# Kernel optimization log

Hardware: AMD Instinct MI355X
Metric: run time of the kernel (lower is better)

Reference implementation:

```python
import jax, jax.numpy as jnp
import numpy as np


def setup_inputs() -> dict:
    key = jax.random.key(0)
    k1, k2, k3, k4, k5 = jax.random.split(key, 5)
    B, T, U, D = 4, 256, 64, 512
    H, V = 512, 1024  # forward_output_size, num_classes
    return {
        "encoder_outputs": jax.random.normal(k1, (B, T, D), dtype=jnp.float32),
        "decoder_outputs": jax.random.normal(k2, (B, U, D), dtype=jnp.float32),
        "w1": jax.random.normal(k3, (H, 2 * D), dtype=jnp.float32) * 0.02,
        "b1": jax.random.normal(k4, (H,), dtype=jnp.float32) * 0.02,
        "w2": jax.random.normal(k5, (V, H), dtype=jnp.float32) * 0.02,
    }


def reference(encoder_outputs, decoder_outputs, w1, b1, w2):
    # Faithful to: concat([enc broadcast to (B,T,U,D), dec broadcast to (B,T,U,D)], -1)
    # -> Linear(w1,b1) -> GELU(tanh) -> Linear(w2, no bias).
    # Linear on the concat equals split-weight projections summed via broadcast
    # (classic RNNT joint decomposition): same math, avoids the (B,T,U,2D) tensor.
    D = encoder_outputs.shape[-1]
    w_enc, w_dec = w1[:, :D], w1[:, D:]
    enc_proj = jnp.einsum("btd,hd->bth", encoder_outputs, w_enc)  # (B,T,H)
    dec_proj = jnp.einsum("bud,hd->buh", decoder_outputs, w_dec)  # (B,U,H)
    hidden = enc_proj[:, :, None, :] + dec_proj[:, None, :, :] + b1  # (B,T,U,H)
    hidden = jax.nn.gelu(hidden, approximate=True)  # tanh approximation, matches nn.GELU('tanh')
    logits = jnp.einsum("btuh,vh->btuv", hidden, w2)  # (B,T,U,V)
    return logits
```

## Files before the change

kernel.cpp:

```cpp
#include <hip/hip_runtime.h>
#include <hip/hip_bf16.h>
#include <stdint.h>


typedef __bf16 bf16_t;
typedef bf16_t bf16x8 __attribute__((ext_vector_type(8)));
typedef float f32x4 __attribute__((ext_vector_type(4)));
typedef unsigned short u16x8 __attribute__((ext_vector_type(8)));

#define GLD16(gp, lp)                                                          \
  __builtin_amdgcn_global_load_lds(                                            \
      (const __attribute__((address_space(1))) void*)(gp),                     \
      (__attribute__((address_space(3))) void*)(lp), 16, 0, 0)

__device__ __forceinline__ unsigned short f2bf(float f) {
  unsigned int u = __float_as_uint(f);
  return (unsigned short)((u + 0x7FFFu + ((u >> 16) & 1u)) >> 16);
}

__device__ __forceinline__ float gelu_f(float x) {
  float t = 1.5957691216057308f * x + 0.07135481283867141f * (x * x * x);
  float e = __expf(-t);
  return x * __builtin_amdgcn_rcpf(1.0f + e);
}

__global__ __launch_bounds__(256) void prep_kernel(
    const float* __restrict__ enc, const float* __restrict__ dec,
    const float* __restrict__ w1, const float* __restrict__ w2,
    unsigned short* __restrict__ o) {
  int i = (blockIdx.x * 256 + threadIdx.x) * 4;
  float4 v;
  if (i < 524288) {
    v = *(const float4*)(enc + i);
  } else if (i < 655360) {
    v = *(const float4*)(dec + (i - 524288));
  } else if (i < 917504) {
    int j = i - 655360;
    v = *(const float4*)(w1 + (j >> 9) * 1024 + (j & 511));
  } else if (i < 1179648) {
    int j = i - 917504;
    v = *(const float4*)(w1 + (j >> 9) * 1024 + 512 + (j & 511));
  } else {
    v = *(const float4*)(w2 + (i - 1179648));
  }
  ushort4 r;
  r.x = f2bf(v.x); r.y = f2bf(v.y); r.z = f2bf(v.z); r.w = f2bf(v.w);
  *(ushort4*)(o + i) = r;
}

__global__ __launch_bounds__(256) void hidden_kernel(
    const float* __restrict__ ep, const float* __restrict__ dp,
    const float* __restrict__ b1, unsigned short* __restrict__ o) {
  int g = blockIdx.x * 256 + threadIdx.x;
  int m = g >> 6;
  int h = (g & 63) << 3;
  int er = m >> 6;
  int dr = ((m >> 14) << 6) | (m & 63);
  float4 e0 = *(const float4*)(ep + er * 512 + h);
  float4 e1 = *(const float4*)(ep + er * 512 + h + 4);
  float4 d0 = *(const float4*)(dp + dr * 512 + h);
  float4 d1 = *(const float4*)(dp + dr * 512 + h + 4);
  float4 b0 = *(const float4*)(b1 + h);
  float4 b1v = *(const float4*)(b1 + h + 4);
  u16x8 r;
  r[0] = f2bf(gelu_f(e0.x + d0.x + b0.x));
  r[1] = f2bf(gelu_f(e0.y + d0.y + b0.y));
  r[2] = f2bf(gelu_f(e0.z + d0.z + b0.z));
  r[3] = f2bf(gelu_f(e0.w + d0.w + b0.w));
  r[4] = f2bf(gelu_f(e1.x + d1.x + b1v.x));
  r[5] = f2bf(gelu_f(e1.y + d1.y + b1v.y));
  r[6] = f2bf(gelu_f(e1.z + d1.z + b1v.z));
  r[7] = f2bf(gelu_f(e1.w + d1.w + b1v.w));
  *(u16x8*)(o + (size_t)g * 8) = r;
}

__device__ __forceinline__ void gemm_core(
    const bf16_t* __restrict__ A, const bf16_t* __restrict__ B,
    float* __restrict__ C, int m0, int n0, int N, int K) {
  __shared__ bf16_t sA[128 * 64];
  __shared__ bf16_t sB[128 * 64];

  const int tid = threadIdx.x;
  const int lane = tid & 63;
  const int w = tid >> 6;
  const int wm = (w >> 1) * 64;
  const int wn = (w & 1) * 64;

  const int srow = w * 32 + (lane >> 3);
  const int scol = (((lane & 7) ^ (lane >> 3)) << 3);
  const bf16_t* gA = A + (size_t)(m0 + srow) * K + scol;
  const bf16_t* gB = B + (size_t)(n0 + srow) * K + scol;

  const int rowA = wm + (lane & 15);
  const int rowB = wn + (lane & 15);
  const int sw0 = (lane >> 4) ^ (lane & 7);
  const bf16x8* pA = (const bf16x8*)sA;
  const bf16x8* pB = (const bf16x8*)sB;

  f32x4 acc[4][4] = {};

  for (int kt = 0; kt < K; kt += 64) {
#pragma unroll
    for (int j = 0; j < 4; j++) {
      GLD16(gA + (size_t)(j * 8) * K + kt, sA + (w * 4 + j) * 512);
      GLD16(gB + (size_t)(j * 8) * K + kt, sB + (w * 4 + j) * 512);
    }
    __syncthreads();

#pragma unroll
    for (int kk = 0; kk < 2; kk++) {
      const int sw = sw0 ^ (kk << 2);
      bf16x8 af[4], bb[4];
#pragma unroll
      for (int i = 0; i < 4; i++) af[i] = pA[(rowA + i * 16) * 8 + sw];
#pragma unroll
      for (int j = 0; j < 4; j++) bb[j] = pB[(rowB + j * 16) * 8 + sw];
#pragma unroll
      for (int i = 0; i < 4; i++)
#pragma unroll
        for (int j = 0; j < 4; j++)
          acc[i][j] = __builtin_amdgcn_mfma_f32_16x16x32_bf16(
              af[i], bb[j], acc[i][j], 0, 0, 0);
    }
    __syncthreads();
  }

  const int crow = m0 + wm + (lane >> 4) * 4;
  const int ccol = n0 + wn + (lane & 15);
  float* Cp = C + (size_t)crow * N + ccol;
#pragma unroll
  for (int i = 0; i < 4; i++)
#pragma unroll
    for (int r = 0; r < 4; r++)
#pragma unroll
      for (int j = 0; j < 4; j++)
        Cp[(size_t)(i * 16 + r) * N + j * 16] = acc[i][j][r];
}

__global__ __launch_bounds__(256) void proj_kernel(
    const bf16_t* __restrict__ encA, const bf16_t* __restrict__ wenc,
    float* __restrict__ encC, const bf16_t* __restrict__ decA,
    const bf16_t* __restrict__ wdec, float* __restrict__ decC) {
  int by = blockIdx.y;
  if (by < 8) {
    gemm_core(encA, wenc, encC, by * 128, blockIdx.x * 128, 512, 512);
  } else {
    gemm_core(decA, wdec, decC, (by - 8) * 128, blockIdx.x * 128, 512, 512);
  }
}


#define STG_A(BUF, RH, KT)                                                     \
  do {                                                                         \
    GLD16(gA + (size_t)((RH) * 64) * 512 + (KT) * 64,                          \
          &sA[BUF][(RH) * 64 + w * 8][0]);                                     \
    GLD16(gA + (size_t)((RH) * 64 + 128) * 512 + (KT) * 64,                    \
          &sA[BUF][(RH) * 64 + 128 + w * 8][0]);                               \
  } while (0)

#define STG_B(BUF, H, KT)                                                      \
  do {                                                                         \
    GLD16(gB + (size_t)((H) * 128) * 512 + (KT) * 64,                          \
          &sB[BUF][(H) * 128 + w * 16][0]);                                    \
    GLD16(gB + (size_t)((H) * 128 + 8) * 512 + (KT) * 64,                      \
          &sB[BUF][(H) * 128 + w * 16 + 8][0]);                                \
  } while (0)

#define RD_A(BUF, F, KK)                                                       \
  pA[(BUF) * 2048 + (rowA + (F) * 16) * 8 + (sw0 ^ ((KK) << 2))]
#define RD_B(BUF, ROFF, KK)                                                    \
  pB[(BUF) * 2048 + (rowB + (ROFF)) * 8 + (sw0 ^ ((KK) << 2))]

#define VMC4 asm volatile("s_waitcnt vmcnt(4)" ::: "memory")
#define VMC0 asm volatile("s_waitcnt vmcnt(0)" ::: "memory")
#define NOPX ((void)0)

#define PHASE(BUF, RH, CH, STAGE, VM)                                          \
  do {                                                                         \
    if ((CH) == 0) {                                                           \
      _Pragma("unroll") for (int f = 0; f < 4; f++) {                          \
        af[f][0] = RD_A(BUF, (RH) * 4 + f, 0);                                 \
        af[f][1] = RD_A(BUF, (RH) * 4 + f, 1);                                 \
      }                                                                        \
    }                                                                          \
    _Pragma("unroll") for (int cf = 0; cf < 2; cf++) {                         \
      bb[cf][0] = RD_B(BUF, (CH) * 128 + cf * 16, 0);                          \
      bb[cf][1] = RD_B(BUF, (CH) * 128 + cf * 16, 1);                          \
    }                                                                          \
    STAGE;                                                                     \
    VM;                                                                        \
    __builtin_amdgcn_s_barrier();                                              \
    __builtin_amdgcn_s_setprio(1);                                             \
    _Pragma("unroll") for (int f = 0; f < 4; f++) {                            \
      _Pragma("unroll") for (int cf = 0; cf < 2; cf++) {                       \
        acc[(RH) * 4 + f][(CH) * 2 + cf] =                                     \
            __builtin_amdgcn_mfma_f32_16x16x32_bf16(                           \
                af[f][0], bb[cf][0], acc[(RH) * 4 + f][(CH) * 2 + cf], 0, 0,   \
                0);                                                            \
        acc[(RH) * 4 + f][(CH) * 2 + cf] =                                     \
            __builtin_amdgcn_mfma_f32_16x16x32_bf16(                           \
                af[f][1], bb[cf][1], acc[(RH) * 4 + f][(CH) * 2 + cf], 0, 0,   \
                0);                                                            \
      }                                                                        \
    }                                                                          \
    __builtin_amdgcn_s_setprio(0);                                             \
    __builtin_amdgcn_s_barrier();                                              \
  } while (0)

__global__ __launch_bounds__(512, 2) void gemm_big2(
    const bf16_t* __restrict__ A, const bf16_t* __restrict__ B,
    float* __restrict__ C) {
  __shared__ bf16_t sA[2][256][64];
  __shared__ bf16_t sB[2][256][64];

  const int tid = threadIdx.x;
  const int lane = tid & 63;
  const int w = tid >> 6;
  const int wr = w >> 2;
  const int wc = w & 3;

  const int bid = blockIdx.x;
  const int swz = (bid & 7) * 128 + (bid >> 3);
  const int m0 = (swz >> 2) * 256;
  const int n0 = (swz & 3) * 256;

  const int srowA = w * 8 + (lane >> 3);
  const int srowB = w * 16 + (lane >> 3);
  const int scol = ((lane & 7) ^ (lane >> 3)) << 3;
  const bf16_t* gA = A + (size_t)(m0 + srowA) * 512 + scol;
  const bf16_t* gB = B + (size_t)(n0 + srowB) * 512 + scol;

  const int rowA = wr * 128 + (lane & 15);
  const int rowB = wc * 32 + (lane & 15);
  const int sw0 = (lane >> 4) ^ (lane & 7);
  const bf16x8* pA = (const bf16x8*)sA;
  const bf16x8* pB = (const bf16x8*)sB;

  f32x4 acc[8][4] = {};
  bf16x8 af[4][2], bb[2][2];

  STG_A(0, 0, 0); STG_B(0, 0, 0); STG_A(0, 1, 0); STG_B(0, 1, 0);
  STG_A(1, 0, 1); STG_B(1, 0, 1);
  VMC4;
  __builtin_amdgcn_s_barrier();

#pragma unroll 1
  for (int i = 0; i < 3; i++) {
    const int t1k = 2 * i + 1;
    const int t2k = 2 * i + 2;
    const int t3k = 2 * i + 3;
    PHASE(0, 0, 0, STG_A(1, 1, t1k), NOPX);
    PHASE(0, 0, 1, STG_B(1, 1, t1k), NOPX);
    PHASE(0, 1, 0, STG_A(0, 0, t2k), NOPX);
    PHASE(0, 1, 1, STG_B(0, 0, t2k), VMC4);
    PHASE(1, 0, 0, STG_A(0, 1, t2k), NOPX);
    PHASE(1, 0, 1, STG_B(0, 1, t2k), NOPX);
    PHASE(1, 1, 0, STG_A(1, 0, t3k), NOPX);
    PHASE(1, 1, 1, STG_B(1, 0, t3k), VMC4);
  }
  PHASE(0, 0, 0, STG_A(1, 1, 7), NOPX);
  PHASE(0, 0, 1, STG_B(1, 1, 7), NOPX);
  PHASE(0, 1, 0, NOPX, NOPX);
  PHASE(0, 1, 1, NOPX, VMC0);
  PHASE(1, 0, 0, NOPX, NOPX);
  PHASE(1, 0, 1, NOPX, NOPX);
  PHASE(1, 1, 0, NOPX, NOPX);
  PHASE(1, 1, 1, NOPX, NOPX);

  const int crow = m0 + wr * 128 + (lane >> 4) * 4;
  const int ccol = n0 + wc * 32 + (lane & 15);
  float* Cp = C + (size_t)crow * 1024 + ccol;
#pragma unroll
  for (int f = 0; f < 8; f++)
#pragma unroll
    for (int r = 0; r < 4; r++)
#pragma unroll
      for (int c = 0; c < 4; c++)
        Cp[(size_t)(f * 16 + r) * 1024 + (c >> 1) * 128 + (c & 1) * 16] =
            acc[f][c][r];
}

extern "C" void kernel_launch(void* const* d_in, const int* in_sizes, int n_in,
                              void* d_out, int out_size, void* d_ws,
                              size_t ws_size, hipStream_t stream) {
  const float* enc = (const float*)d_in[0];
  const float* dec = (const float*)d_in[1];
  const float* w1  = (const float*)d_in[2];
  const float* b1  = (const float*)d_in[3];
  const float* w2  = (const float*)d_in[4];
  float* out = (float*)d_out;

  unsigned short* bf      = (unsigned short*)d_ws;
  unsigned short* ws_enc  = bf;
  unsigned short* ws_dec  = bf + 524288;
  unsigned short* ws_wenc = bf + 655360;
  unsigned short* ws_wdec = bf + 917504;
  unsigned short* ws_w2   = bf + 1179648;
  float* encp = (float*)((char*)d_ws + 3407872);
  float* decp = encp + 524288;
  unsigned short* hid = (unsigned short*)(decp + 131072);

  prep_kernel<<<1664, 256, 0, stream>>>(enc, dec, w1, w2, bf);

  proj_kernel<<<dim3(4, 10), 256, 0, stream>>>(
      (const bf16_t*)ws_enc, (const bf16_t*)ws_wenc, encp,
      (const bf16_t*)ws_dec, (const bf16_t*)ws_wdec, decp);

  hidden_kernel<<<16384, 256, 0, stream>>>(encp, decp, b1, hid);

  gemm_big2<<<1024, 512, 0, stream>>>(
      (const bf16_t*)hid, (const bf16_t*)ws_w2, out);
}
```

Before: 362.4 us.

## Fuse broadcast-add GELU hidden computation into the big GEMM's A-tile staging

```diff
diff --git a/kernel.cpp b/kernel.cpp
--- a/kernel.cpp
+++ b/kernel.cpp
@@ -48,35 +48,10 @@
   *(ushort4*)(o + i) = r;
 }
 
-__global__ __launch_bounds__(256) void hidden_kernel(
-    const float* __restrict__ ep, const float* __restrict__ dp,
-    const float* __restrict__ b1, unsigned short* __restrict__ o) {
-  int g = blockIdx.x * 256 + threadIdx.x;
-  int m = g >> 6;
-  int h = (g & 63) << 3;
-  int er = m >> 6;
-  int dr = ((m >> 14) << 6) | (m & 63);
-  float4 e0 = *(const float4*)(ep + er * 512 + h);
-  float4 e1 = *(const float4*)(ep + er * 512 + h + 4);
-  float4 d0 = *(const float4*)(dp + dr * 512 + h);
-  float4 d1 = *(const float4*)(dp + dr * 512 + h + 4);
-  float4 b0 = *(const float4*)(b1 + h);
-  float4 b1v = *(const float4*)(b1 + h + 4);
-  u16x8 r;
-  r[0] = f2bf(gelu_f(e0.x + d0.x + b0.x));
-  r[1] = f2bf(gelu_f(e0.y + d0.y + b0.y));
-  r[2] = f2bf(gelu_f(e0.z + d0.z + b0.z));
-  r[3] = f2bf(gelu_f(e0.w + d0.w + b0.w));
-  r[4] = f2bf(gelu_f(e1.x + d1.x + b1v.x));
-  r[5] = f2bf(gelu_f(e1.y + d1.y + b1v.y));
-  r[6] = f2bf(gelu_f(e1.z + d1.z + b1v.z));
-  r[7] = f2bf(gelu_f(e1.w + d1.w + b1v.w));
-  *(u16x8*)(o + (size_t)g * 8) = r;
-}
-
 __device__ __forceinline__ void gemm_core(
     const bf16_t* __restrict__ A, const bf16_t* __restrict__ B,
-    float* __restrict__ C, int m0, int n0, int N, int K) {
+    float* __restrict__ C, int m0, int n0, int N, int K,
+    const float* __restrict__ bias) {
   __shared__ bf16_t sA[128 * 64];
   __shared__ bf16_t sB[128 * 64];
 
@@ -127,6 +102,11 @@
 
   const int crow = m0 + wm + (lane >> 4) * 4;
   const int ccol = n0 + wn + (lane & 15);
+  float bvs[4] = {0.f, 0.f, 0.f, 0.f};
+  if (bias) {
+#pragma unroll
+    for (int j = 0; j < 4; j++) bvs[j] = bias[ccol + j * 16];
+  }
   float* Cp = C + (size_t)crow * N + ccol;
 #pragma unroll
   for (int i = 0; i < 4; i++)
@@ -134,28 +114,68 @@
     for (int r = 0; r < 4; r++)
 #pragma unroll
       for (int j = 0; j < 4; j++)
-        Cp[(size_t)(i * 16 + r) * N + j * 16] = acc[i][j][r];
+        Cp[(size_t)(i * 16 + r) * N + j * 16] = acc[i][j][r] + bvs[j];
 }
 
 __global__ __launch_bounds__(256) void proj_kernel(
     const bf16_t* __restrict__ encA, const bf16_t* __restrict__ wenc,
     float* __restrict__ encC, const bf16_t* __restrict__ decA,
-    const bf16_t* __restrict__ wdec, float* __restrict__ decC) {
+    const bf16_t* __restrict__ wdec, float* __restrict__ decC,
+    const float* __restrict__ b1) {
   int by = blockIdx.y;
   if (by < 8) {
-    gemm_core(encA, wenc, encC, by * 128, blockIdx.x * 128, 512, 512);
+    gemm_core(encA, wenc, encC, by * 128, blockIdx.x * 128, 512, 512, b1);
   } else {
-    gemm_core(decA, wdec, decC, (by - 8) * 128, blockIdx.x * 128, 512, 512);
+    gemm_core(decA, wdec, decC, (by - 8) * 128, blockIdx.x * 128, 512, 512,
+              nullptr);
   }
 }
 
 
 #define STG_A(BUF, RH, KT)                                                     \
   do {                                                                         \
-    GLD16(gA + (size_t)((RH) * 64) * 512 + (KT) * 64,                          \
-          &sA[BUF][(RH) * 64 + w * 8][0]);                                     \
-    GLD16(gA + (size_t)((RH) * 64 + 128) * 512 + (KT) * 64,                    \
-          &sA[BUF][(RH) * 64 + 128 + w * 8][0]);                               \
+    const int rl_ = tid >> 2;                                                  \
+    const int row_ = (RH) * 64 + (rl_ & 63) + ((rl_ >> 6) << 7);               \
+    const int mm_ = m0 + row_;                                                 \
+    const int co_ = ((tid & 3) << 4) + (KT) * 64;                              \
+    const float* ep_ = epb + ((size_t)(mm_ >> 6) << 9) + co_;                  \
+    const float* dp_ =                                                         \
+        dpq + ((size_t)(((mm_ >> 14) << 6) | (mm_ & 63)) << 9) + co_;          \
+    u16x8* dst_ = ((u16x8*)&sA[0][0][0]) + (BUF) * 2048 + row_ * 8;            \
+    const int sl_ = (tid & 3) << 1;                                            \
+    const int rx_ = row_ & 7;                                                  \
+    {                                                                          \
+      float4 e0_ = *(const float4*)(ep_);                                      \
+      float4 e1_ = *(const float4*)(ep_ + 4);                                  \
+      float4 d0_ = *(const float4*)(dp_);                                      \
+      float4 d1_ = *(const float4*)(dp_ + 4);                                  \
+      u16x8 h_;                                                                \
+      h_[0] = f2bf(gelu_f(e0_.x + d0_.x));                                     \
+      h_[1] = f2bf(gelu_f(e0_.y + d0_.y));                                     \
+      h_[2] = f2bf(gelu_f(e0_.z + d0_.z));                                     \
+      h_[3] = f2bf(gelu_f(e0_.w + d0_.w));                                     \
+      h_[4] = f2bf(gelu_f(e1_.x + d1_.x));                                     \
+      h_[5] = f2bf(gelu_f(e1_.y + d1_.y));                                     \
+      h_[6] = f2bf(gelu_f(e1_.z + d1_.z));                                     \
+      h_[7] = f2bf(gelu_f(e1_.w + d1_.w));                                     \
+      dst_[sl_ ^ rx_] = h_;                                                    \
+    }                                                                          \
+    {                                                                          \
+      float4 e2_ = *(const float4*)(ep_ + 8);                                  \
+      float4 e3_ = *(const float4*)(ep_ + 12);                                 \
+      float4 d2_ = *(const float4*)(dp_ + 8);                                  \
+      float4 d3_ = *(const float4*)(dp_ + 12);                                 \
+      u16x8 h_;                                                                \
+      h_[0] = f2bf(gelu_f(e2_.x + d2_.x));                                     \
+      h_[1] = f2bf(gelu_f(e2_.y + d2_.y));                                     \
+      h_[2] = f2bf(gelu_f(e2_.z + d2_.z));                                     \
+      h_[3] = f2bf(gelu_f(e2_.w + d2_.w));                                     \
+      h_[4] = f2bf(gelu_f(e3_.x + d3_.x));                                     \
+      h_[5] = f2bf(gelu_f(e3_.y + d3_.y));                                     \
+      h_[6] = f2bf(gelu_f(e3_.z + d3_.z));                                     \
+      h_[7] = f2bf(gelu_f(e3_.w + d3_.w));                                     \
+      dst_[(sl_ + 1) ^ rx_] = h_;                                              \
+    }                                                                          \
   } while (0)
 
 #define STG_B(BUF, H, KT)                                                      \
@@ -171,11 +191,12 @@
 #define RD_B(BUF, ROFF, KK)                                                    \
   pB[(BUF) * 2048 + (rowB + (ROFF)) * 8 + (sw0 ^ ((KK) << 2))]
 
-#define VMC4 asm volatile("s_waitcnt vmcnt(4)" ::: "memory")
+#define VMC2 asm volatile("s_waitcnt vmcnt(2)" ::: "memory")
 #define VMC0 asm volatile("s_waitcnt vmcnt(0)" ::: "memory")
+#define ALGK asm volatile("s_waitcnt lgkmcnt(0)" ::: "memory")
 #define NOPX ((void)0)
 
-#define PHASE(BUF, RH, CH, STAGE, VM)                                          \
+#define PHASE(BUF, RH, CH, STAGE, FENCE)                                       \
   do {                                                                         \
     if ((CH) == 0) {                                                           \
       _Pragma("unroll") for (int f = 0; f < 4; f++) {                          \
@@ -188,7 +209,7 @@
       bb[cf][1] = RD_B(BUF, (CH) * 128 + cf * 16, 1);                          \
     }                                                                          \
     STAGE;                                                                     \
-    VM;                                                                        \
+    FENCE;                                                                     \
     __builtin_amdgcn_s_barrier();                                              \
     __builtin_amdgcn_s_setprio(1);                                             \
     _Pragma("unroll") for (int f = 0; f < 4; f++) {                            \
@@ -204,12 +225,11 @@
       }                                                                        \
     }                                                                          \
     __builtin_amdgcn_s_setprio(0);                                             \
-    __builtin_amdgcn_s_barrier();                                              \
   } while (0)
 
-__global__ __launch_bounds__(512, 2) void gemm_big2(
-    const bf16_t* __restrict__ A, const bf16_t* __restrict__ B,
-    float* __restrict__ C) {
+__global__ __launch_bounds__(512, 2) void gemm_fused(
+    const float* __restrict__ epb, const float* __restrict__ dpq,
+    const bf16_t* __restrict__ B, float* __restrict__ C) {
   __shared__ bf16_t sA[2][256][64];
   __shared__ bf16_t sB[2][256][64];
 
@@ -224,10 +244,8 @@
   const int m0 = (swz >> 2) * 256;
   const int n0 = (swz & 3) * 256;
 
-  const int srowA = w * 8 + (lane >> 3);
   const int srowB = w * 16 + (lane >> 3);
   const int scol = ((lane & 7) ^ (lane >> 3)) << 3;
-  const bf16_t* gA = A + (size_t)(m0 + srowA) * 512 + scol;
   const bf16_t* gB = B + (size_t)(n0 + srowB) * 512 + scol;
 
   const int rowA = wr * 128 + (lane & 15);
@@ -239,9 +257,12 @@
   f32x4 acc[8][4] = {};
   bf16x8 af[4][2], bb[2][2];
 
-  STG_A(0, 0, 0); STG_B(0, 0, 0); STG_A(0, 1, 0); STG_B(0, 1, 0);
-  STG_A(1, 0, 1); STG_B(1, 0, 1);
-  VMC4;
+  STG_B(0, 0, 0); STG_B(0, 1, 0);
+  STG_A(0, 0, 0); STG_A(0, 1, 0);
+  STG_A(1, 0, 1);
+  STG_B(1, 0, 1);
+  VMC2;
+  ALGK;
   __builtin_amdgcn_s_barrier();
 
 #pragma unroll 1
@@ -249,16 +270,16 @@
     const int t1k = 2 * i + 1;
     const int t2k = 2 * i + 2;
     const int t3k = 2 * i + 3;
-    PHASE(0, 0, 0, STG_A(1, 1, t1k), NOPX);
+    PHASE(0, 0, 0, STG_A(1, 1, t1k), ALGK);
     PHASE(0, 0, 1, STG_B(1, 1, t1k), NOPX);
-    PHASE(0, 1, 0, STG_A(0, 0, t2k), NOPX);
-    PHASE(0, 1, 1, STG_B(0, 0, t2k), VMC4);
-    PHASE(1, 0, 0, STG_A(0, 1, t2k), NOPX);
+    PHASE(0, 1, 0, STG_A(0, 0, t2k), ALGK);
+    PHASE(0, 1, 1, STG_B(0, 0, t2k), VMC2);
+    PHASE(1, 0, 0, STG_A(0, 1, t2k), ALGK);
     PHASE(1, 0, 1, STG_B(0, 1, t2k), NOPX);
-    PHASE(1, 1, 0, STG_A(1, 0, t3k), NOPX);
-    PHASE(1, 1, 1, STG_B(1, 0, t3k), VMC4);
-  }
-  PHASE(0, 0, 0, STG_A(1, 1, 7), NOPX);
+    PHASE(1, 1, 0, STG_A(1, 0, t3k), ALGK);
+    PHASE(1, 1, 1, STG_B(1, 0, t3k), VMC2);
+  }
+  PHASE(0, 0, 0, STG_A(1, 1, 7), ALGK);
   PHASE(0, 0, 1, STG_B(1, 1, 7), NOPX);
   PHASE(0, 1, 0, NOPX, NOPX);
   PHASE(0, 1, 1, NOPX, VMC0);
@@ -298,16 +319,13 @@
   unsigned short* ws_w2   = bf + 1179648;
   float* encp = (float*)((char*)d_ws + 3407872);
   float* decp = encp + 524288;
-  unsigned short* hid = (unsigned short*)(decp + 131072);
 
   prep_kernel<<<1664, 256, 0, stream>>>(enc, dec, w1, w2, bf);
 
   proj_kernel<<<dim3(4, 10), 256, 0, stream>>>(
       (const bf16_t*)ws_enc, (const bf16_t*)ws_wenc, encp,
-      (const bf16_t*)ws_dec, (const bf16_t*)ws_wdec, decp);
-
-  hidden_kernel<<<16384, 256, 0, stream>>>(encp, decp, b1, hid);
-
-  gemm_big2<<<1024, 512, 0, stream>>>(
-      (const bf16_t*)hid, (const bf16_t*)ws_w2, out);
-}
+      (const bf16_t*)ws_dec, (const bf16_t*)ws_wdec, decp, b1);
+
+  gemm_fused<<<1024, 512, 0, stream>>>(
+      encp, decp, (const bf16_t*)ws_w2, out);
+}
```

After: 392.6 us. 8.3% more time.
